# Kernel optimization log

Measured on AMD Instinct MI355X. Metric: run time of the kernel, lower is better.

The kernel has to match this reference:

```python
import jax, jax.numpy as jnp
import numpy as np

KH = KW = 3  # kernel spatial size is hard-coded to 3 in the original layer


def _tdiv2(x):
    # matches tf.cast(x / 2, tf.int32): true-divide by 2, truncate toward zero
    return jnp.trunc(x * 0.5)


def setup_inputs() -> dict:
    key = jax.random.key(0)
    k1, k2, k3 = jax.random.split(key, 3)
    B, H, W, C, F = 4, 32, 32, 64, 128
    # integer-valued tensors stored as float32 (bit-serial math needs integer weights)
    inputs = jax.random.randint(k1, (B, H, W, C), 0, 16).astype(jnp.float32)
    kernel = jax.random.randint(k2, (KH, KW, C, F), -8, 8).astype(jnp.float32)
    bias = jax.random.randint(k3, (F,), -4, 4).astype(jnp.float32)
    return {"inputs": inputs, "kernel": kernel, "bias": bias, "bits": 4}


def reference(inputs, kernel, bias, bits):
    # Bit-serial conv2d, padding='same' (pad=1), activation='relu'.
    # Per (kernel position, input element, output channel) the original computes
    #   acc <- trunc((acc + x * (w mod 2) * sign(w_orig)) / 2); w <- trunc(w / 2)
    # for `bits` iterations, then sums over channels/kernel window.
    B, H, W, C = inputs.shape
    F = kernel.shape[-1]
    x = jnp.pad(inputs, ((0, 0), (1, 1), (1, 1), (0, 0)))  # 'same' padding, pad=1
    out = jnp.zeros((B, H, W, F), inputs.dtype)
    for i in range(KH):
        for j in range(KW):
            patch = x[:, i:i + H, j:j + W, :][..., None]   # [B,H,W,C,1]
            w = kernel[i, j]                               # [C,F]
            s = jnp.sign(w)                                # sign of ORIGINAL weight, fixed
            acc = jnp.zeros((B, H, W, C, F), inputs.dtype)
            ww = w
            for _ in range(bits):
                acc = _tdiv2(acc + patch * (jnp.mod(ww, 2.0) * s))
                ww = _tdiv2(ww)
            out = out + acc.sum(axis=3)                    # sum over C; kernel window summed by loop
    return jax.nn.relu(out + bias)
```

## Files before the change

### kernel.cpp

```cpp
#include <hip/hip_runtime.h>
#include <stdint.h>


#define NWPK 36864
#define XOFF 36864
#define NXPK 147968

static __device__ __forceinline__ int pk_mad_i16(int a, int b, int c) {
    int d;
    asm("v_pk_mad_i16 %0, %1, %2, %3" : "=v"(d) : "v"(a), "v"(b), "v"(c));
    return d;
}
static __device__ __forceinline__ int pk_ashr(int sh, int a) {
    int d;
    asm("v_pk_ashrrev_i16 %0, %1, %2" : "=v"(d) : "v"(sh), "v"(a));
    return d;
}
static __device__ __forceinline__ int pk_add_i16(int a, int b) {
    int d;
    asm("v_pk_add_i16 %0, %1, %2" : "=v"(d) : "v"(a), "v"(b));
    return d;
}

__global__ __launch_bounds__(256) void prep_all(const float* __restrict__ kern,
                                                const float* __restrict__ input,
                                                uint32_t* __restrict__ ws) {
    int bid = blockIdx.x, tid = threadIdx.x;
    if (bid < 144) {
        int t  = bid * 256 + tid;
        int u  = t & 3;
        int f  = (t >> 2) & 127;
        int cq = (t >> 9) & 3;
        int gk = t >> 11;
        int g  = gk & 1;
        int ki = gk >> 1;
        int c  = cq * 16 + g * 8 + u * 2;
        int wlo = (int)kern[(ki * 64 + c    ) * 128 + f];
        int whi = (int)kern[(ki * 64 + c + 1) * 128 + f];
        ws[t] = (uint32_t)(uint16_t)(int16_t)wlo |
                ((uint32_t)(uint16_t)(int16_t)whi << 16);
    } else {
        int t = (bid - 144) * 256 + tid;
        if (t >= NXPK) return;
        int c2    = t & 31;
        int rest  = t >> 5;
        int wp    = rest % 34;
        int rest2 = rest / 34;
        int hp    = rest2 % 34;
        int b     = rest2 / 34;
        int v = 0;
        if (hp >= 1 && hp <= 32 && wp >= 1 && wp <= 32) {
            const float* p = &input[(((b * 32) + hp - 1) * 32 + (wp - 1)) * 64 + c2 * 2];
            v = (int)p[0] | ((int)p[1] << 16);
        }
        ws[XOFF + t] = (uint32_t)v;
    }
}

__global__ __launch_bounds__(512, 4) void conv_main(const uint32_t* __restrict__ ws,
                                                    const float* __restrict__ bias,
                                                    float* __restrict__ out) {
    const uint32_t* xpk = ws + XOFF;

    int bid = blockIdx.x;
    int wq  = bid & 7;
    int h   = (bid >> 3) & 31;
    int b   = bid >> 8;
    int tid = threadIdx.x;
    int f   = tid & 127;
    int cq  = tid >> 7;
    int w0  = wq * 4;

    __shared__ uint32_t xl[3 * 6 * 32];
    __shared__ int prt[4 * 4 * 128];

    #pragma unroll
    for (int pass = 0; pass < 2; ++pass) {
        int k = pass * 512 + tid;
        if (k < 576) {
            int c2  = k & 31;
            int rc  = k >> 5;
            int col = rc % 6;
            int r   = rc / 6;
            xl[k] = xpk[((b * 34 + h + r) * 34 + (w0 + col)) * 32 + c2];
        }
    }

    int4 wv[18];
    const int4* wp = (const int4*)ws;
    #pragma unroll
    for (int i = 0; i < 18; ++i) wv[i] = wp[i * 512 + tid];

    __syncthreads();

    const int SH4  = 0x00040004;
    const int SH15 = 0x000F000F;
    int acc0 = 0, acc1 = 0, acc2 = 0, acc3 = 0;

    #pragma unroll
    for (int row = 0; row < 3; ++row) {
        #pragma unroll
        for (int g = 0; g < 2; ++g) {
            const uint32_t* xb = xl + (row * 6) * 32 + cq * 8 + g * 4;
            int4 xc[6];
            #pragma unroll
            for (int cidx = 0; cidx < 6; ++cidx)
                xc[cidx] = *(const int4*)(xb + cidx * 32);
            #pragma unroll
            for (int j = 0; j < 3; ++j) {
                const int4 w4 = wv[(row * 3 + j) * 2 + g];
                #pragma unroll
                for (int u = 0; u < 4; ++u) {
                    int w2 = (&w4.x)[u];
                    int A  = pk_ashr(SH15, w2) & 0x000F000F;
                    acc0 = pk_add_i16(acc0, pk_ashr(SH4, pk_mad_i16((&xc[j + 0].x)[u], w2, A)));
                    acc1 = pk_add_i16(acc1, pk_ashr(SH4, pk_mad_i16((&xc[j + 1].x)[u], w2, A)));
                    acc2 = pk_add_i16(acc2, pk_ashr(SH4, pk_mad_i16((&xc[j + 2].x)[u], w2, A)));
                    acc3 = pk_add_i16(acc3, pk_ashr(SH4, pk_mad_i16((&xc[j + 3].x)[u], w2, A)));
                }
            }
        }
    }

    prt[(cq * 4 + 0) * 128 + f] = (int)(short)(acc0 & 0xffff) + (acc0 >> 16);
    prt[(cq * 4 + 1) * 128 + f] = (int)(short)(acc1 & 0xffff) + (acc1 >> 16);
    prt[(cq * 4 + 2) * 128 + f] = (int)(short)(acc2 & 0xffff) + (acc2 >> 16);
    prt[(cq * 4 + 3) * 128 + f] = (int)(short)(acc3 & 0xffff) + (acc3 >> 16);
    __syncthreads();

    {
        int ff = tid & 127;
        int px = tid >> 7;
        int v = prt[(0 * 4 + px) * 128 + ff] + prt[(1 * 4 + px) * 128 + ff] +
                prt[(2 * 4 + px) * 128 + ff] + prt[(3 * 4 + px) * 128 + ff] +
                (int)bias[ff];
        out[((b * 32 + h) * 32 + w0 + px) * 128 + ff] = (float)(v < 0 ? 0 : v);
    }
}

extern "C" void kernel_launch(void* const* d_in, const int* in_sizes, int n_in,
                              void* d_out, int out_size, void* d_ws, size_t ws_size,
                              hipStream_t stream) {
    const float* input  = (const float*)d_in[0];
    const float* kernel = (const float*)d_in[1];
    const float* bias   = (const float*)d_in[2];

    uint32_t* ws = (uint32_t*)d_ws;

    prep_all<<<144 + 579, 256, 0, stream>>>(kernel, input, ws);
    conv_main<<<1024, 512, 0, stream>>>(ws, bias, (float*)d_out);
}
```

Before: 79.80 us.

## Split output channels across two blocks and spread input channels over eight groups

Each block now handles half of the output filters (64), and the 512 threads are split into 8 channel groups of 8 channels instead of 4 groups of 16. This halves per-thread weight registers (9 int4 instead of 18) and doubles the grid to 2048 blocks, which should improve occupancy and parallelism. The cost is that each block loads the same input tile twice across the two filter halves, and the reduction over channel groups now sums 8 partials, done by half the threads.

```diff
diff --git a/kernel.cpp b/kernel.cpp
--- a/kernel.cpp
+++ b/kernel.cpp
@@ -2,7 +2,6 @@
 #include <stdint.h>
 
 
-#define NWPK 36864
 #define XOFF 36864
 #define NXPK 147968
 
@@ -27,14 +26,16 @@
                                                 uint32_t* __restrict__ ws) {
     int bid = blockIdx.x, tid = threadIdx.x;
     if (bid < 144) {
-        int t  = bid * 256 + tid;
-        int u  = t & 3;
-        int f  = (t >> 2) & 127;
-        int cq = (t >> 9) & 3;
-        int gk = t >> 11;
-        int g  = gk & 1;
-        int ki = gk >> 1;
-        int c  = cq * 16 + g * 8 + u * 2;
+        int t    = bid * 256 + tid;
+        int u    = t & 3;
+        int rest = t >> 2;
+        int f64  = rest & 63;
+        int ce   = (rest >> 6) & 7;
+        int kifh = rest >> 9;
+        int fh   = kifh & 1;
+        int ki   = kifh >> 1;
+        int c    = ce * 8 + u * 2;
+        int f    = fh * 64 + f64;
         int wlo = (int)kern[(ki * 64 + c    ) * 128 + f];
         int whi = (int)kern[(ki * 64 + c + 1) * 128 + f];
         ws[t] = (uint32_t)(uint16_t)(int16_t)wlo |
@@ -63,16 +64,17 @@
     const uint32_t* xpk = ws + XOFF;
 
     int bid = blockIdx.x;
-    int wq  = bid & 7;
-    int h   = (bid >> 3) & 31;
-    int b   = bid >> 8;
+    int fh  = bid & 1;
+    int wq  = (bid >> 1) & 7;
+    int h   = (bid >> 4) & 31;
+    int b   = bid >> 9;
     int tid = threadIdx.x;
-    int f   = tid & 127;
-    int cq  = tid >> 7;
+    int f64 = tid & 63;
+    int ce  = tid >> 6;
     int w0  = wq * 4;
 
     __shared__ uint32_t xl[3 * 6 * 32];
-    __shared__ int prt[4 * 4 * 128];
+    __shared__ int prt[8 * 4 * 64];
 
     #pragma unroll
     for (int pass = 0; pass < 2; ++pass) {
@@ -86,10 +88,10 @@
         }
     }
 
-    int4 wv[18];
-    const int4* wp = (const int4*)ws;
+    int4 wv[9];
+    const int4* wp4 = (const int4*)ws;
     #pragma unroll
-    for (int i = 0; i < 18; ++i) wv[i] = wp[i * 512 + tid];
+    for (int ki = 0; ki < 9; ++ki) wv[ki] = wp4[(ki * 2 + fh) * 512 + tid];
 
     __syncthreads();
 
@@ -99,42 +101,41 @@
 
     #pragma unroll
     for (int row = 0; row < 3; ++row) {
+        const uint32_t* xb = xl + (row * 6) * 32 + ce * 4;
+        int4 xc[6];
         #pragma unroll
-        for (int g = 0; g < 2; ++g) {
-            const uint32_t* xb = xl + (row * 6) * 32 + cq * 8 + g * 4;
-            int4 xc[6];
+        for (int cidx = 0; cidx < 6; ++cidx)
+            xc[cidx] = *(const int4*)(xb + cidx * 32);
+        #pragma unroll
+        for (int j = 0; j < 3; ++j) {
+            const int4 w4 = wv[row * 3 + j];
             #pragma unroll
-            for (int cidx = 0; cidx < 6; ++cidx)
-                xc[cidx] = *(const int4*)(xb + cidx * 32);
-            #pragma unroll
-            for (int j = 0; j < 3; ++j) {
-                const int4 w4 = wv[(row * 3 + j) * 2 + g];
-                #pragma unroll
-                for (int u = 0; u < 4; ++u) {
-                    int w2 = (&w4.x)[u];
-                    int A  = pk_ashr(SH15, w2) & 0x000F000F;
-                    acc0 = pk_add_i16(acc0, pk_ashr(SH4, pk_mad_i16((&xc[j + 0].x)[u], w2, A)));
-                    acc1 = pk_add_i16(acc1, pk_ashr(SH4, pk_mad_i16((&xc[j + 1].x)[u], w2, A)));
-                    acc2 = pk_add_i16(acc2, pk_ashr(SH4, pk_mad_i16((&xc[j + 2].x)[u], w2, A)));
-                    acc3 = pk_add_i16(acc3, pk_ashr(SH4, pk_mad_i16((&xc[j + 3].x)[u], w2, A)));
-                }
+            for (int u = 0; u < 4; ++u) {
+                int w2 = (&w4.x)[u];
+                int A  = pk_ashr(SH15, w2) & 0x000F000F;
+                acc0 = pk_add_i16(acc0, pk_ashr(SH4, pk_mad_i16((&xc[j + 0].x)[u], w2, A)));
+                acc1 = pk_add_i16(acc1, pk_ashr(SH4, pk_mad_i16((&xc[j + 1].x)[u], w2, A)));
+                acc2 = pk_add_i16(acc2, pk_ashr(SH4, pk_mad_i16((&xc[j + 2].x)[u], w2, A)));
+                acc3 = pk_add_i16(acc3, pk_ashr(SH4, pk_mad_i16((&xc[j + 3].x)[u], w2, A)));
             }
         }
     }
 
-    prt[(cq * 4 + 0) * 128 + f] = (int)(short)(acc0 & 0xffff) + (acc0 >> 16);
-    prt[(cq * 4 + 1) * 128 + f] = (int)(short)(acc1 & 0xffff) + (acc1 >> 16);
-    prt[(cq * 4 + 2) * 128 + f] = (int)(short)(acc2 & 0xffff) + (acc2 >> 16);
-    prt[(cq * 4 + 3) * 128 + f] = (int)(short)(acc3 & 0xffff) + (acc3 >> 16);
+    prt[(ce * 4 + 0) * 64 + f64] = (int)(short)(acc0 & 0xffff) + (acc0 >> 16);
+    prt[(ce * 4 + 1) * 64 + f64] = (int)(short)(acc1 & 0xffff) + (acc1 >> 16);
+    prt[(ce * 4 + 2) * 64 + f64] = (int)(short)(acc2 & 0xffff) + (acc2 >> 16);
+    prt[(ce * 4 + 3) * 64 + f64] = (int)(short)(acc3 & 0xffff) + (acc3 >> 16);
     __syncthreads();
 
-    {
-        int ff = tid & 127;
-        int px = tid >> 7;
-        int v = prt[(0 * 4 + px) * 128 + ff] + prt[(1 * 4 + px) * 128 + ff] +
-                prt[(2 * 4 + px) * 128 + ff] + prt[(3 * 4 + px) * 128 + ff] +
-                (int)bias[ff];
-        out[((b * 32 + h) * 32 + w0 + px) * 128 + ff] = (float)(v < 0 ? 0 : v);
+    if (tid < 256) {
+        int ff = tid & 63;
+        int px = tid >> 6;
+        int v = 0;
+        #pragma unroll
+        for (int e = 0; e < 8; ++e) v += prt[(e * 4 + px) * 64 + ff];
+        v += (int)bias[fh * 64 + ff];
+        out[((b * 32 + h) * 32 + w0 + px) * 128 + fh * 64 + ff] =
+            (float)(v < 0 ? 0 : v);
     }
 }
 
@@ -148,5 +149,5 @@
     uint32_t* ws = (uint32_t*)d_ws;
 
     prep_all<<<144 + 579, 256, 0, stream>>>(kernel, input, ws);
-    conv_main<<<1024, 512, 0, stream>>>(ws, bias, (float*)d_out);
+    conv_main<<<2048, 512, 0, stream>>>(ws, bias, (float*)d_out);
 }
```

New measurement: 79.67 us. About the same (-0.2%).
